# Performance work log

Hardware: AMD Instinct MI355X
Metric: run time of the kernel (lower is better)

The kernel has to match this reference:

```python
import jax, jax.numpy as jnp
import numpy as np

EPS = 1e-6  # flax nnx LayerNorm default

def _ln(x):
    # LayerNorm without scale/bias
    m = jnp.mean(x, axis=-1, keepdims=True)
    v = jnp.mean(jnp.square(x - m), axis=-1, keepdims=True)
    return (x - m) * jax.lax.rsqrt(v + EPS)

def _modulate(x, shift, scale):
    return x * (1.0 + scale[:, None]) + shift[:, None]

def setup_inputs() -> dict:
    key = jax.random.key(0)
    B, S, H, NH = 8, 1024, 1024, 16
    ks = jax.random.split(key, 12)
    s = lambda k, sh: jax.random.normal(k, sh, dtype=jnp.float32) * 0.02
    return {
        "x": jax.random.normal(ks[0], (B, S, H), dtype=jnp.float32),
        "c": jax.random.normal(ks[1], (B, H), dtype=jnp.float32),
        "w_ada": s(ks[2], (H, 6 * H)),
        "b_ada": jnp.zeros((6 * H,), dtype=jnp.float32),
        "w_qkv": s(ks[3], (H, 3 * H)),
        "w_proj": s(ks[4], (H, H)),
        "b_proj": jnp.zeros((H,), dtype=jnp.float32),
        "w_mlp1": s(ks[5], (H, 4 * H)),
        "b_mlp1": jnp.zeros((4 * H,), dtype=jnp.float32),
        "w_mlp2": s(ks[6], (4 * H, H)),
        "b_mlp2": jnp.zeros((H,), dtype=jnp.float32),
    }

def reference(x, c, w_ada, b_ada, w_qkv, w_proj, b_proj, w_mlp1, b_mlp1, w_mlp2, b_mlp2):
    B, S, H = x.shape
    NH = 16
    CH = H // NH
    # adaLN modulation: silu -> Linear
    cmod = jax.nn.silu(c) @ w_ada + b_ada  # [B, 6H]
    shift_msa, scale_msa, gate_msa, shift_mlp, scale_mlp, gate_mlp = jnp.split(cmod, 6, axis=-1)
    # attention branch
    x_mod = _modulate(_ln(x), shift_msa, scale_msa)
    qkv = x_mod @ w_qkv  # [B, S, 3H]
    k, q, v = jnp.split(qkv, 3, axis=-1)  # note source order: k, q, v
    k = k.reshape(B, S, NH, CH)
    q = q.reshape(B, S, NH, CH)
    v = v.reshape(B, S, NH, CH)
    q = q / CH  # faithful: divide by head_dim (not sqrt)
    w = jnp.einsum('bqhc,bkhc->bhqk', q, k).astype(jnp.float32)
    w = jax.nn.softmax(w, axis=-1)
    y = jnp.einsum('bhqk,bkhc->bqhc', w, v).reshape(B, S, H)
    attn_x = y @ w_proj + b_proj
    x = x + gate_msa[:, None] * attn_x
    # MLP branch
    x_mod2 = _modulate(_ln(x), shift_mlp, scale_mlp)
    h = jax.nn.gelu(x_mod2 @ w_mlp1 + b_mlp1)
    mlp_x = h @ w_mlp2 + b_mlp2
    x = x + gate_mlp[:, None] * mlp_x
    return x
```

## Files before the change

kernel.cpp:

```cpp
#include <hip/hip_runtime.h>
#include <stdint.h>

typedef unsigned short u16;
using bf16x8 = __attribute__((ext_vector_type(8))) __bf16;
using f32x4  = __attribute__((ext_vector_type(4))) float;

#define MFMA16(a,b,c) __builtin_amdgcn_mfma_f32_16x16x32_bf16((a),(b),(c),0,0,0)

__device__ __forceinline__ u16 f2bf(float f) {
  union { float f; uint32_t u; } v; v.f = f;
  uint32_t r = v.u + 0x7FFFu + ((v.u >> 16) & 1u);
  return (u16)(r >> 16);
}

__device__ __forceinline__ void gload_lds16(const void* g, void* l) {
  typedef const __attribute__((address_space(1))) void* gp_t;
  typedef __attribute__((address_space(3))) void* lp_t;
  __builtin_amdgcn_global_load_lds((gp_t)(uintptr_t)g,
                                   (lp_t)(uint32_t)(uintptr_t)l, 16, 0, 0);
}

__global__ __launch_bounds__(256)
void adaln_part_k(const float* __restrict__ c, const float* __restrict__ w,
                  float* __restrict__ partial) {
  const int jb = blockIdx.x, ks = blockIdx.y;
  const int j = jb * 256 + threadIdx.x;
  __shared__ float sil[8][32];
  {
    int b = threadIdx.x >> 5, kk = threadIdx.x & 31;
    float v = c[b * 1024 + ks * 32 + kk];
    sil[b][kk] = v / (1.f + __expf(-v));
  }
  __syncthreads();
  float acc[8] = {0,0,0,0,0,0,0,0};
#pragma unroll 8
  for (int kk = 0; kk < 32; ++kk) {
    float wv = w[(size_t)(ks * 32 + kk) * 6144 + j];
#pragma unroll
    for (int b = 0; b < 8; ++b) acc[b] += sil[b][kk] * wv;
  }
#pragma unroll
  for (int b = 0; b < 8; ++b)
    partial[((size_t)ks * 8 + b) * 6144 + j] = acc[b];
}

__global__ __launch_bounds__(256)
void adaln_red_k(const float* __restrict__ partial, const float* __restrict__ bias,
                 float* __restrict__ cmod) {
  int g = blockIdx.x * 256 + threadIdx.x;
  int j = g % 6144;
  float s = bias[j];
#pragma unroll 8
  for (int ks = 0; ks < 32; ++ks)
    s += partial[(size_t)ks * 8 * 6144 + g];
  cmod[g] = s;
}

__global__ __launch_bounds__(256)
void tcast_k(const float* __restrict__ in, u16* __restrict__ out, int K, int N,
             int lo, int hi, float scale) {
  __shared__ u16 t[64][65];
  int n0 = blockIdx.x * 64, k0 = blockIdx.y * 64;
#pragma unroll
  for (int i = 0; i < 16; ++i) {
    int idx = i * 256 + threadIdx.x;
    int r = idx >> 6, cc = idx & 63;
    float v = in[(size_t)(k0 + r) * N + n0 + cc];
    int n = n0 + cc;
    if (n >= lo && n < hi) v *= scale;
    t[r][cc] = f2bf(v);
  }
  __syncthreads();
#pragma unroll
  for (int i = 0; i < 16; ++i) {
    int idx = i * 256 + threadIdx.x;
    int r = idx >> 6, cc = idx & 63;
    out[(size_t)(n0 + r) * K + k0 + cc] = t[cc][r];
  }
}

__global__ __launch_bounds__(256)
void lnmod_k(const float* __restrict__ x, const float* __restrict__ cmod,
             int shift_off, int scale_off, u16* __restrict__ out) {
  int row = blockIdx.x;
  int b = row >> 10;
  const float4* xr = (const float4*)(x + (size_t)row * 1024);
  float4 v = xr[threadIdx.x];
  float s = v.x + v.y + v.z + v.w;
  float sq = v.x * v.x + v.y * v.y + v.z * v.z + v.w * v.w;
#pragma unroll
  for (int m = 32; m >= 1; m >>= 1) {
    s  += __shfl_xor(s, m);
    sq += __shfl_xor(sq, m);
  }
  __shared__ float ss[4], ssq[4];
  int wave = threadIdx.x >> 6, lane = threadIdx.x & 63;
  if (lane == 0) { ss[wave] = s; ssq[wave] = sq; }
  __syncthreads();
  s  = ss[0] + ss[1] + ss[2] + ss[3];
  sq = ssq[0] + ssq[1] + ssq[2] + ssq[3];
  float mean = s * (1.f / 1024.f);
  float var  = sq * (1.f / 1024.f) - mean * mean;
  float rstd = rsqrtf(var + 1e-6f);
  int col = threadIdx.x * 4;
  const float* sh = cmod + (size_t)b * 6144 + shift_off + col;
  const float* sc = cmod + (size_t)b * 6144 + scale_off + col;
  float xv[4] = {v.x, v.y, v.z, v.w};
  union { u16 o[4]; uint64_t u; } pk;
#pragma unroll
  for (int j = 0; j < 4; ++j)
    pk.o[j] = f2bf((xv[j] - mean) * rstd * (1.f + sc[j]) + sh[j]);
  *(uint64_t*)(out + (size_t)row * 1024 + col) = pk.u;
}

__global__ __launch_bounds__(256)
void tv_k(const u16* __restrict__ qkv, u16* __restrict__ vt) {
  __shared__ u16 t[64][65];
  int r0 = blockIdx.x * 64;
  int h = blockIdx.y;
  int b = r0 >> 10;
  int s0 = r0 & 1023;
#pragma unroll
  for (int i = 0; i < 16; ++i) {
    int idx = i * 256 + threadIdx.x;
    int r = idx >> 6, cc = idx & 63;
    t[r][cc] = qkv[(size_t)(r0 + r) * 3072 + 2048 + h * 64 + cc];
  }
  __syncthreads();
#pragma unroll
  for (int i = 0; i < 16; ++i) {
    int idx = i * 256 + threadIdx.x;
    int ch = idx >> 6, scc = idx & 63;
    vt[((size_t)(b * 16 + h) * 64 + ch) * 1024 + s0 + scc] = t[scc][ch];
  }
}

__device__ __forceinline__ float gelu_f(float x) {
  float z = 1.5957691216057308f * (x + 0.044715f * x * x * x);
  return x / (1.f + __expf(-z));
}

template <int EP>
__global__ __launch_bounds__(256)
void gemm_k(const u16* __restrict__ A, const u16* __restrict__ Bt,
            int N, int K,
            const float* __restrict__ bias, const float* __restrict__ resid,
            const float* __restrict__ gate, void* __restrict__ outp) {
  __shared__ __align__(16) u16 lds[2][2][128 * 32];
  const int nwg = gridDim.x * gridDim.y;
  int bid = blockIdx.y * gridDim.x + blockIdx.x;
  int swz = (bid & 7) * (nwg >> 3) + (bid >> 3);
  const int bn = swz % gridDim.x, bm = swz / gridDim.x;
  const int tid = threadIdx.x;
  const int wave = tid >> 6, lane = tid & 63;
  const int l15 = lane & 15, lhi = lane >> 4;
  const int wr = wave >> 1, wc = wave & 1;
  f32x4 acc[4][4] = {};
  const int nkt = K >> 5;
  const size_t arow0 = (size_t)bm * 128;
  const size_t brow0 = (size_t)bn * 128;

  auto stage = [&](int buf, int kt) {
#pragma unroll
    for (int i = 0; i < 2; ++i) {
      int c = (i * 4 + wave) * 64 + lane;
      int row = c >> 2;
      int kc = (c & 3) ^ ((row >> 1) & 3);
      gload_lds16(A  + (arow0 + row) * K + (size_t)kt * 32 + kc * 8,
                  &lds[buf][0][(i * 4 + wave) * 512]);
      gload_lds16(Bt + (brow0 + row) * K + (size_t)kt * 32 + kc * 8,
                  &lds[buf][1][(i * 4 + wave) * 512]);
    }
  };

  stage(0, 0);
  __syncthreads();
  for (int kt = 0; kt < nkt; ++kt) {
    int cur = kt & 1;
    if (kt + 1 < nkt) stage(cur ^ 1, kt + 1);
    bf16x8 af[4], bfr[4];
#pragma unroll
    for (int m = 0; m < 4; ++m) {
      int r = wr * 64 + m * 16 + l15;
      af[m] = *(const bf16x8*)&lds[cur][0][r * 32 + (lhi ^ ((r >> 1) & 3)) * 8];
    }
#pragma unroll
    for (int n = 0; n < 4; ++n) {
      int r = wc * 64 + n * 16 + l15;
      bfr[n] = *(const bf16x8*)&lds[cur][1][r * 32 + (lhi ^ ((r >> 1) & 3)) * 8];
    }
#pragma unroll
    for (int m = 0; m < 4; ++m)
#pragma unroll
      for (int n = 0; n < 4; ++n)
        acc[m][n] = MFMA16(af[m], bfr[n], acc[m][n]);
    __syncthreads();
  }

#pragma unroll
  for (int m = 0; m < 4; ++m) {
    int row = bm * 128 + wr * 64 + m * 16 + lhi * 4;
#pragma unroll
    for (int n = 0; n < 4; ++n) {
      int col = bn * 128 + wc * 64 + n * 16 + l15;
#pragma unroll
      for (int r = 0; r < 4; ++r) {
        int rr = row + r;
        float v = acc[m][n][r];
        if (EP == 0) {
          ((u16*)outp)[(size_t)rr * N + col] = f2bf(v);
        } else if (EP == 1) {
          ((u16*)outp)[(size_t)rr * N + col] = f2bf(gelu_f(v + bias[col]));
        } else {
          float t = v + bias[col];
          int b = rr >> 10;
          float res = resid[(size_t)rr * N + col];
          ((float*)outp)[(size_t)rr * N + col] = res + gate[(size_t)b * 6144 + col] * t;
        }
      }
    }
  }
}

__global__ __launch_bounds__(256)
void attn_k(const u16* __restrict__ qkv, const u16* __restrict__ vt,
            u16* __restrict__ y) {
  int bid0 = blockIdx.x + 16 * (blockIdx.y + 16 * blockIdx.z);
  int swz = (bid0 & 7) * 256 + (bid0 >> 3);
  const int qt = swz & 15, h = (swz >> 4) & 15, b = swz >> 8;
  const int tid = threadIdx.x, wave = tid >> 6, lane = tid & 63;
  const int l15 = lane & 15, lhi = lane >> 4;
  __shared__ __align__(16) u16 Qs[64 * 64];
  __shared__ __align__(16) u16 Ks[2][64 * 64];
  __shared__ __align__(16) u16 Vs[2][64 * 64];
  __shared__ __align__(16) u16 Ps[64 * 64];
  const size_t qrow0 = (size_t)b * 1024 + qt * 64;
  const size_t krow0 = (size_t)b * 1024;
  const size_t vrow0 = (size_t)(b * 16 + h) * 64;

  auto stageQ = [&]() {
#pragma unroll
    for (int i = 0; i < 2; ++i) {
      int c = (i * 4 + wave) * 64 + lane;
      int r = c >> 3, j = (c & 7) ^ (c >> 3 & 7);
      gload_lds16(qkv + (qrow0 + r) * 3072 + 1024 + h * 64 + j * 8,
                  &Qs[(i * 4 + wave) * 512]);
    }
  };
  auto stageKV = [&](int buf, int kt) {
#pragma unroll
    for (int i = 0; i < 2; ++i) {
      int c = (i * 4 + wave) * 64 + lane;
      int r = c >> 3, j = (c & 7) ^ (c >> 3 & 7);
      gload_lds16(qkv + (krow0 + kt * 64 + r) * 3072 + h * 64 + j * 8,
                  &Ks[buf][(i * 4 + wave) * 512]);
      gload_lds16(vt + (vrow0 + r) * 1024 + kt * 64 + j * 8,
                  &Vs[buf][(i * 4 + wave) * 512]);
    }
  };
  auto ldb = [](const u16* base, int row, int cc) -> bf16x8 {
    return *(const bf16x8*)&base[row * 64 + ((cc ^ (row & 7)) << 3)];
  };

  stageQ();
  stageKV(0, 0);
  __syncthreads();
  bf16x8 qf[2];
  qf[0] = ldb(Qs, wave * 16 + l15, lhi);
  qf[1] = ldb(Qs, wave * 16 + l15, 4 + lhi);

  bf16x8 ones;
#pragma unroll
  for (int j = 0; j < 8; ++j) ones[j] = (__bf16)1.0f;

  float m_r[4];
  f32x4 o[5] = {};
#pragma unroll
  for (int r = 0; r < 4; ++r) m_r[r] = -3.0e38f;

  for (int kt = 0; kt < 16; ++kt) {
    int cur = kt & 1;
    if (kt < 15) stageKV(cur ^ 1, kt + 1);
    f32x4 sf[4] = {};
    __builtin_amdgcn_s_setprio(1);
#pragma unroll
    for (int n = 0; n < 4; ++n) {
      bf16x8 k0 = ldb(Ks[cur], n * 16 + l15, lhi);
      bf16x8 k1 = ldb(Ks[cur], n * 16 + l15, 4 + lhi);
      sf[n] = MFMA16(qf[0], k0, sf[n]);
      sf[n] = MFMA16(qf[1], k1, sf[n]);
    }
    __builtin_amdgcn_s_setprio(0);
#pragma unroll
    for (int r = 0; r < 4; ++r) {
      float mx = fmaxf(fmaxf(sf[0][r], sf[1][r]), fmaxf(sf[2][r], sf[3][r]));
      mx = fmaxf(mx, __shfl_xor(mx, 1));
      mx = fmaxf(mx, __shfl_xor(mx, 2));
      mx = fmaxf(mx, __shfl_xor(mx, 4));
      mx = fmaxf(mx, __shfl_xor(mx, 8));
      float mn = fmaxf(m_r[r], mx);
      float al = __expf(m_r[r] - mn);
      m_r[r] = mn;
      float p0 = __expf(sf[0][r] - mn);
      float p1 = __expf(sf[1][r] - mn);
      float p2 = __expf(sf[2][r] - mn);
      float p3 = __expf(sf[3][r] - mn);
      o[0][r] *= al; o[1][r] *= al; o[2][r] *= al; o[3][r] *= al; o[4][r] *= al;
      int row = wave * 16 + lhi * 4 + r;
      int rb = row * 64, sw = (row & 7) << 3;
      Ps[rb + (l15 ^ sw)]        = f2bf(p0);
      Ps[rb + ((l15 + 16) ^ sw)] = f2bf(p1);
      Ps[rb + ((l15 + 32) ^ sw)] = f2bf(p2);
      Ps[rb + ((l15 + 48) ^ sw)] = f2bf(p3);
    }
    bf16x8 pf0 = ldb(Ps, wave * 16 + l15, lhi);
    bf16x8 pf1 = ldb(Ps, wave * 16 + l15, 4 + lhi);
    __builtin_amdgcn_s_setprio(1);
#pragma unroll
    for (int n = 0; n < 4; ++n) {
      bf16x8 v0 = ldb(Vs[cur], n * 16 + l15, lhi);
      bf16x8 v1 = ldb(Vs[cur], n * 16 + l15, 4 + lhi);
      o[n] = MFMA16(pf0, v0, o[n]);
      o[n] = MFMA16(pf1, v1, o[n]);
    }
    o[4] = MFMA16(pf0, ones, o[4]);
    o[4] = MFMA16(pf1, ones, o[4]);
    __builtin_amdgcn_s_setprio(0);
    __syncthreads();
  }
#pragma unroll
  for (int r = 0; r < 4; ++r) {
    float inv = 1.0f / o[4][r];
    size_t yrow = (qrow0 + wave * 16 + lhi * 4 + r) * 1024 + h * 64 + l15;
    y[yrow]      = f2bf(o[0][r] * inv);
    y[yrow + 16] = f2bf(o[1][r] * inv);
    y[yrow + 32] = f2bf(o[2][r] * inv);
    y[yrow + 48] = f2bf(o[3][r] * inv);
  }
}

extern "C" void kernel_launch(void* const* d_in, const int* in_sizes, int n_in,
                              void* d_out, int out_size, void* d_ws, size_t ws_size,
                              hipStream_t stream) {
  const float* x      = (const float*)d_in[0];
  const float* c      = (const float*)d_in[1];
  const float* w_ada  = (const float*)d_in[2];
  const float* b_ada  = (const float*)d_in[3];
  const float* w_qkv  = (const float*)d_in[4];
  const float* w_proj = (const float*)d_in[5];
  const float* b_proj = (const float*)d_in[6];
  const float* w_mlp1 = (const float*)d_in[7];
  const float* b_mlp1 = (const float*)d_in[8];
  const float* w_mlp2 = (const float*)d_in[9];
  const float* b_mlp2 = (const float*)d_in[10];
  float* out = (float*)d_out;

  char* ws = (char*)d_ws;
  size_t off = 0;
  auto alloc = [&](size_t bytes) {
    void* p = ws + off;
    off += (bytes + 255) & ~(size_t)255;
    return p;
  };
  float* cmod  = (float*)alloc((size_t)8 * 6144 * 4);
  float* apart = (float*)alloc((size_t)32 * 8 * 6144 * 4);
  u16* wqkvT   = (u16*)alloc((size_t)3072 * 1024 * 2);
  u16* wprojT  = (u16*)alloc((size_t)1024 * 1024 * 2);
  u16* wmlp1T  = (u16*)alloc((size_t)4096 * 1024 * 2);
  u16* wmlp2T  = (u16*)alloc((size_t)1024 * 4096 * 2);
  u16* xmod    = (u16*)alloc((size_t)8192 * 1024 * 2);
  u16* qkv     = (u16*)alloc((size_t)8192 * 3072 * 2);
  u16* vt      = (u16*)alloc((size_t)8 * 16 * 64 * 1024 * 2);
  float* x1    = (float*)alloc((size_t)8192 * 1024 * 4);
  u16* hbuf    = (u16*)alloc((size_t)8192 * 4096 * 2);
  u16* ybuf  = xmod;
  u16* xmod2 = qkv;

  adaln_part_k<<<dim3(24, 32), 256, 0, stream>>>(c, w_ada, apart);
  adaln_red_k<<<192, 256, 0, stream>>>(apart, b_ada, cmod);
  tcast_k<<<dim3(3072 / 64, 1024 / 64), 256, 0, stream>>>(w_qkv,  wqkvT,  1024, 3072,
                                                          1024, 2048, 1.0f / 64.0f);
  tcast_k<<<dim3(1024 / 64, 1024 / 64), 256, 0, stream>>>(w_proj, wprojT, 1024, 1024, 0, 0, 1.f);
  tcast_k<<<dim3(4096 / 64, 1024 / 64), 256, 0, stream>>>(w_mlp1, wmlp1T, 1024, 4096, 0, 0, 1.f);
  tcast_k<<<dim3(1024 / 64, 4096 / 64), 256, 0, stream>>>(w_mlp2, wmlp2T, 4096, 1024, 0, 0, 1.f);
  lnmod_k<<<8192, 256, 0, stream>>>(x, cmod, 0, 1024, xmod);
  gemm_k<0><<<dim3(3072 / 128, 8192 / 128), 256, 0, stream>>>(
      xmod, wqkvT, 3072, 1024, nullptr, nullptr, nullptr, qkv);
  tv_k<<<dim3(128, 16), 256, 0, stream>>>(qkv, vt);
  attn_k<<<dim3(16, 16, 8), 256, 0, stream>>>(qkv, vt, ybuf);
  gemm_k<2><<<dim3(1024 / 128, 8192 / 128), 256, 0, stream>>>(
      ybuf, wprojT, 1024, 1024, b_proj, x, cmod + 2048, x1);
  lnmod_k<<<8192, 256, 0, stream>>>(x1, cmod, 3072, 4096, xmod2);
  gemm_k<1><<<dim3(4096 / 128, 8192 / 128), 256, 0, stream>>>(
      xmod2, wmlp1T, 4096, 1024, b_mlp1, nullptr, nullptr, hbuf);
  gemm_k<2><<<dim3(1024 / 128, 8192 / 128), 256, 0, stream>>>(
      hbuf, wmlp2T, 1024, 4096, b_mlp2, x1, cmod + 5120, out);
}
```

Before: 409.4 us.

## Add 256x128 tile GEMM kernel for QKV and MLP GEMMs, drop block swizzle

Adds a gemm2_k variant in which each 256-thread block computes a 256x128 output tile, each wave holding 8x4 MFMA accumulators. It is used for the QKV, MLP1 and MLP2 GEMMs. The goal is more arithmetic per byte of LDS traffic, better operand reuse, and fewer blocks. The grouped block-index swizzle is also removed from the original gemm_k, so tiles launch in plain row-major order, which may hurt L2 locality. The larger tile raises register pressure (launch_bounds 256,2) and halves the block count, which could reduce occupancy or leave part of the GPU idle for the smaller N=1024 GEMM.

```diff
diff --git a/kernel.cpp b/kernel.cpp
--- a/kernel.cpp
+++ b/kernel.cpp
@@ -141,16 +141,99 @@
 }
 
 template <int EP>
+__global__ __launch_bounds__(256, 2)
+void gemm2_k(const u16* __restrict__ A, const u16* __restrict__ Bt,
+             int N, int K,
+             const float* __restrict__ bias, const float* __restrict__ resid,
+             const float* __restrict__ gate, void* __restrict__ outp) {
+  __shared__ __align__(16) u16 As[2][256 * 32];
+  __shared__ __align__(16) u16 Bs[2][128 * 32];
+  const int bn = blockIdx.x, bm = blockIdx.y;
+  const int tid = threadIdx.x;
+  const int wave = tid >> 6, lane = tid & 63;
+  const int l15 = lane & 15, lhi = lane >> 4;
+  const int wr = wave >> 1, wc = wave & 1;
+  f32x4 acc[8][4] = {};
+  const int nkt = K >> 5;
+  const size_t arow0 = (size_t)bm * 256;
+  const size_t brow0 = (size_t)bn * 128;
+
+  auto stage = [&](int buf, int kt) {
+#pragma unroll
+    for (int i = 0; i < 4; ++i) {
+      int q = (i * 4 + wave) * 64 + lane;
+      int row = q >> 2;
+      int kc = (q & 3) ^ ((row >> 1) & 3);
+      gload_lds16(A + (arow0 + row) * K + (size_t)kt * 32 + kc * 8,
+                  &As[buf][(i * 4 + wave) * 512]);
+    }
+#pragma unroll
+    for (int i = 0; i < 2; ++i) {
+      int q = (i * 4 + wave) * 64 + lane;
+      int row = q >> 2;
+      int kc = (q & 3) ^ ((row >> 1) & 3);
+      gload_lds16(Bt + (brow0 + row) * K + (size_t)kt * 32 + kc * 8,
+                  &Bs[buf][(i * 4 + wave) * 512]);
+    }
+  };
+
+  stage(0, 0);
+  __syncthreads();
+  for (int kt = 0; kt < nkt; ++kt) {
+    int cur = kt & 1;
+    if (kt + 1 < nkt) stage(cur ^ 1, kt + 1);
+    bf16x8 af[8], bfr[4];
+#pragma unroll
+    for (int m = 0; m < 8; ++m) {
+      int r = wr * 128 + m * 16 + l15;
+      af[m] = *(const bf16x8*)&As[cur][r * 32 + (lhi ^ ((r >> 1) & 3)) * 8];
+    }
+#pragma unroll
+    for (int n = 0; n < 4; ++n) {
+      int r = wc * 64 + n * 16 + l15;
+      bfr[n] = *(const bf16x8*)&Bs[cur][r * 32 + (lhi ^ ((r >> 1) & 3)) * 8];
+    }
+#pragma unroll
+    for (int m = 0; m < 8; ++m)
+#pragma unroll
+      for (int n = 0; n < 4; ++n)
+        acc[m][n] = MFMA16(af[m], bfr[n], acc[m][n]);
+    __syncthreads();
+  }
+
+#pragma unroll
+  for (int m = 0; m < 8; ++m) {
+    int row = bm * 256 + wr * 128 + m * 16 + lhi * 4;
+#pragma unroll
+    for (int n = 0; n < 4; ++n) {
+      int col = bn * 128 + wc * 64 + n * 16 + l15;
+#pragma unroll
+      for (int r = 0; r < 4; ++r) {
+        int rr = row + r;
+        float v = acc[m][n][r];
+        if (EP == 0) {
+          ((u16*)outp)[(size_t)rr * N + col] = f2bf(v);
+        } else if (EP == 1) {
+          ((u16*)outp)[(size_t)rr * N + col] = f2bf(gelu_f(v + bias[col]));
+        } else {
+          float t = v + bias[col];
+          int b = rr >> 10;
+          float res = resid[(size_t)rr * N + col];
+          ((float*)outp)[(size_t)rr * N + col] = res + gate[(size_t)b * 6144 + col] * t;
+        }
+      }
+    }
+  }
+}
+
+template <int EP>
 __global__ __launch_bounds__(256)
 void gemm_k(const u16* __restrict__ A, const u16* __restrict__ Bt,
             int N, int K,
             const float* __restrict__ bias, const float* __restrict__ resid,
             const float* __restrict__ gate, void* __restrict__ outp) {
   __shared__ __align__(16) u16 lds[2][2][128 * 32];
-  const int nwg = gridDim.x * gridDim.y;
-  int bid = blockIdx.y * gridDim.x + blockIdx.x;
-  int swz = (bid & 7) * (nwg >> 3) + (bid >> 3);
-  const int bn = swz % gridDim.x, bm = swz / gridDim.x;
+  const int bn = blockIdx.x, bm = blockIdx.y;
   const int tid = threadIdx.x;
   const int wave = tid >> 6, lane = tid & 63;
   const int l15 = lane & 15, lhi = lane >> 4;
@@ -384,15 +467,15 @@
   tcast_k<<<dim3(4096 / 64, 1024 / 64), 256, 0, stream>>>(w_mlp1, wmlp1T, 1024, 4096, 0, 0, 1.f);
   tcast_k<<<dim3(1024 / 64, 4096 / 64), 256, 0, stream>>>(w_mlp2, wmlp2T, 4096, 1024, 0, 0, 1.f);
   lnmod_k<<<8192, 256, 0, stream>>>(x, cmod, 0, 1024, xmod);
-  gemm_k<0><<<dim3(3072 / 128, 8192 / 128), 256, 0, stream>>>(
+  gemm2_k<0><<<dim3(3072 / 128, 8192 / 256), 256, 0, stream>>>(
       xmod, wqkvT, 3072, 1024, nullptr, nullptr, nullptr, qkv);
   tv_k<<<dim3(128, 16), 256, 0, stream>>>(qkv, vt);
   attn_k<<<dim3(16, 16, 8), 256, 0, stream>>>(qkv, vt, ybuf);
   gemm_k<2><<<dim3(1024 / 128, 8192 / 128), 256, 0, stream>>>(
       ybuf, wprojT, 1024, 1024, b_proj, x, cmod + 2048, x1);
   lnmod_k<<<8192, 256, 0, stream>>>(x1, cmod, 3072, 4096, xmod2);
-  gemm_k<1><<<dim3(4096 / 128, 8192 / 128), 256, 0, stream>>>(
+  gemm2_k<1><<<dim3(4096 / 128, 8192 / 256), 256, 0, stream>>>(
       xmod2, wmlp1T, 4096, 1024, b_mlp1, nullptr, nullptr, hbuf);
-  gemm_k<2><<<dim3(1024 / 128, 8192 / 128), 256, 0, stream>>>(
+  gemm2_k<2><<<dim3(1024 / 128, 8192 / 256), 256, 0, stream>>>(
       hbuf, wmlp2T, 1024, 4096, b_mlp2, x1, cmod + 5120, out);
 }
```

Measured after the change: 435.3 us. +6.3%, slower.

## Double attention query tile to 128 rows per block to reuse K/V tiles

Applied to the files above, without the earlier changes.

The attention kernel now processes 128 query rows per block (two 16-row groups per wave) instead of 64, halving the grid and the number of times each K/V tile is loaded from global memory into LDS. Each K/V tile staged into shared memory is reused across twice as many query rows, cutting global/L2 traffic and barrier count per unit of work. In exchange, register use (two sets of accumulators and softmax state) and LDS grow, and the grid shrinks to 1024 blocks, which may lower occupancy or latency hiding.

```diff
diff --git a/kernel.cpp b/kernel.cpp
--- a/kernel.cpp
+++ b/kernel.cpp
@@ -225,33 +225,33 @@
 __global__ __launch_bounds__(256)
 void attn_k(const u16* __restrict__ qkv, const u16* __restrict__ vt,
             u16* __restrict__ y) {
-  int bid0 = blockIdx.x + 16 * (blockIdx.y + 16 * blockIdx.z);
-  int swz = (bid0 & 7) * 256 + (bid0 >> 3);
-  const int qt = swz & 15, h = (swz >> 4) & 15, b = swz >> 8;
+  int bid0 = blockIdx.x + 8 * (blockIdx.y + 16 * blockIdx.z);
+  int swz = (bid0 & 7) * 128 + (bid0 >> 3);
+  const int qt = swz & 7, h = (swz >> 3) & 15, b = swz >> 7;
   const int tid = threadIdx.x, wave = tid >> 6, lane = tid & 63;
   const int l15 = lane & 15, lhi = lane >> 4;
-  __shared__ __align__(16) u16 Qs[64 * 64];
+  __shared__ __align__(16) u16 Qs[128 * 64];
   __shared__ __align__(16) u16 Ks[2][64 * 64];
   __shared__ __align__(16) u16 Vs[2][64 * 64];
-  __shared__ __align__(16) u16 Ps[64 * 64];
-  const size_t qrow0 = (size_t)b * 1024 + qt * 64;
+  __shared__ __align__(16) u16 Ps[128 * 64];
+  const size_t qrow0 = (size_t)b * 1024 + qt * 128;
   const size_t krow0 = (size_t)b * 1024;
   const size_t vrow0 = (size_t)(b * 16 + h) * 64;
 
   auto stageQ = [&]() {
 #pragma unroll
+    for (int i = 0; i < 4; ++i) {
+      int c = (i * 4 + wave) * 64 + lane;
+      int r = c >> 3, j = (c & 7) ^ (r & 7);
+      gload_lds16(qkv + (qrow0 + r) * 3072 + 1024 + h * 64 + j * 8,
+                  &Qs[(i * 4 + wave) * 512]);
+    }
+  };
+  auto stageKV = [&](int buf, int kt) {
+#pragma unroll
     for (int i = 0; i < 2; ++i) {
       int c = (i * 4 + wave) * 64 + lane;
-      int r = c >> 3, j = (c & 7) ^ (c >> 3 & 7);
-      gload_lds16(qkv + (qrow0 + r) * 3072 + 1024 + h * 64 + j * 8,
-                  &Qs[(i * 4 + wave) * 512]);
-    }
-  };
-  auto stageKV = [&](int buf, int kt) {
-#pragma unroll
-    for (int i = 0; i < 2; ++i) {
-      int c = (i * 4 + wave) * 64 + lane;
-      int r = c >> 3, j = (c & 7) ^ (c >> 3 & 7);
+      int r = c >> 3, j = (c & 7) ^ (r & 7);
       gload_lds16(qkv + (krow0 + kt * 64 + r) * 3072 + h * 64 + j * 8,
                   &Ks[buf][(i * 4 + wave) * 512]);
       gload_lds16(vt + (vrow0 + r) * 1024 + kt * 64 + j * 8,
@@ -265,78 +265,90 @@
   stageQ();
   stageKV(0, 0);
   __syncthreads();
-  bf16x8 qf[2];
-  qf[0] = ldb(Qs, wave * 16 + l15, lhi);
-  qf[1] = ldb(Qs, wave * 16 + l15, 4 + lhi);
+  bf16x8 qf[2][2];
+#pragma unroll
+  for (int g = 0; g < 2; ++g) {
+    int r = wave * 32 + g * 16 + l15;
+    qf[g][0] = ldb(Qs, r, lhi);
+    qf[g][1] = ldb(Qs, r, 4 + lhi);
+  }
 
   bf16x8 ones;
 #pragma unroll
   for (int j = 0; j < 8; ++j) ones[j] = (__bf16)1.0f;
 
-  float m_r[4];
-  f32x4 o[5] = {};
-#pragma unroll
-  for (int r = 0; r < 4; ++r) m_r[r] = -3.0e38f;
+  float m_r[2][4];
+  f32x4 o[2][5] = {};
+#pragma unroll
+  for (int g = 0; g < 2; ++g)
+#pragma unroll
+    for (int r = 0; r < 4; ++r) m_r[g][r] = -3.0e38f;
 
   for (int kt = 0; kt < 16; ++kt) {
     int cur = kt & 1;
     if (kt < 15) stageKV(cur ^ 1, kt + 1);
-    f32x4 sf[4] = {};
-    __builtin_amdgcn_s_setprio(1);
-#pragma unroll
-    for (int n = 0; n < 4; ++n) {
-      bf16x8 k0 = ldb(Ks[cur], n * 16 + l15, lhi);
-      bf16x8 k1 = ldb(Ks[cur], n * 16 + l15, 4 + lhi);
-      sf[n] = MFMA16(qf[0], k0, sf[n]);
-      sf[n] = MFMA16(qf[1], k1, sf[n]);
-    }
-    __builtin_amdgcn_s_setprio(0);
+#pragma unroll
+    for (int g = 0; g < 2; ++g) {
+      f32x4 sf[4] = {};
+      __builtin_amdgcn_s_setprio(1);
+#pragma unroll
+      for (int n = 0; n < 4; ++n) {
+        bf16x8 k0 = ldb(Ks[cur], n * 16 + l15, lhi);
+        bf16x8 k1 = ldb(Ks[cur], n * 16 + l15, 4 + lhi);
+        sf[n] = MFMA16(qf[g][0], k0, sf[n]);
+        sf[n] = MFMA16(qf[g][1], k1, sf[n]);
+      }
+      __builtin_amdgcn_s_setprio(0);
+#pragma unroll
+      for (int r = 0; r < 4; ++r) {
+        float mx = fmaxf(fmaxf(sf[0][r], sf[1][r]), fmaxf(sf[2][r], sf[3][r]));
+        mx = fmaxf(mx, __shfl_xor(mx, 1));
+        mx = fmaxf(mx, __shfl_xor(mx, 2));
+        mx = fmaxf(mx, __shfl_xor(mx, 4));
+        mx = fmaxf(mx, __shfl_xor(mx, 8));
+        float mn = fmaxf(m_r[g][r], mx);
+        float al = __expf(m_r[g][r] - mn);
+        m_r[g][r] = mn;
+        float p0 = __expf(sf[0][r] - mn);
+        float p1 = __expf(sf[1][r] - mn);
+        float p2 = __expf(sf[2][r] - mn);
+        float p3 = __expf(sf[3][r] - mn);
+        o[g][0][r] *= al; o[g][1][r] *= al; o[g][2][r] *= al;
+        o[g][3][r] *= al; o[g][4][r] *= al;
+        int row = wave * 32 + g * 16 + lhi * 4 + r;
+        int rb = row * 64, sw = (row & 7) << 3;
+        Ps[rb + (l15 ^ sw)]        = f2bf(p0);
+        Ps[rb + ((l15 + 16) ^ sw)] = f2bf(p1);
+        Ps[rb + ((l15 + 32) ^ sw)] = f2bf(p2);
+        Ps[rb + ((l15 + 48) ^ sw)] = f2bf(p3);
+      }
+      bf16x8 pf0 = ldb(Ps, wave * 32 + g * 16 + l15, lhi);
+      bf16x8 pf1 = ldb(Ps, wave * 32 + g * 16 + l15, 4 + lhi);
+      __builtin_amdgcn_s_setprio(1);
+#pragma unroll
+      for (int n = 0; n < 4; ++n) {
+        bf16x8 v0 = ldb(Vs[cur], n * 16 + l15, lhi);
+        bf16x8 v1 = ldb(Vs[cur], n * 16 + l15, 4 + lhi);
+        o[g][n] = MFMA16(pf0, v0, o[g][n]);
+        o[g][n] = MFMA16(pf1, v1, o[g][n]);
+      }
+      o[g][4] = MFMA16(pf0, ones, o[g][4]);
+      o[g][4] = MFMA16(pf1, ones, o[g][4]);
+      __builtin_amdgcn_s_setprio(0);
+    }
+    __syncthreads();
+  }
+#pragma unroll
+  for (int g = 0; g < 2; ++g)
 #pragma unroll
     for (int r = 0; r < 4; ++r) {
-      float mx = fmaxf(fmaxf(sf[0][r], sf[1][r]), fmaxf(sf[2][r], sf[3][r]));
-      mx = fmaxf(mx, __shfl_xor(mx, 1));
-      mx = fmaxf(mx, __shfl_xor(mx, 2));
-      mx = fmaxf(mx, __shfl_xor(mx, 4));
-      mx = fmaxf(mx, __shfl_xor(mx, 8));
-      float mn = fmaxf(m_r[r], mx);
-      float al = __expf(m_r[r] - mn);
-      m_r[r] = mn;
-      float p0 = __expf(sf[0][r] - mn);
-      float p1 = __expf(sf[1][r] - mn);
-      float p2 = __expf(sf[2][r] - mn);
-      float p3 = __expf(sf[3][r] - mn);
-      o[0][r] *= al; o[1][r] *= al; o[2][r] *= al; o[3][r] *= al; o[4][r] *= al;
-      int row = wave * 16 + lhi * 4 + r;
-      int rb = row * 64, sw = (row & 7) << 3;
-      Ps[rb + (l15 ^ sw)]        = f2bf(p0);
-      Ps[rb + ((l15 + 16) ^ sw)] = f2bf(p1);
-      Ps[rb + ((l15 + 32) ^ sw)] = f2bf(p2);
-      Ps[rb + ((l15 + 48) ^ sw)] = f2bf(p3);
-    }
-    bf16x8 pf0 = ldb(Ps, wave * 16 + l15, lhi);
-    bf16x8 pf1 = ldb(Ps, wave * 16 + l15, 4 + lhi);
-    __builtin_amdgcn_s_setprio(1);
-#pragma unroll
-    for (int n = 0; n < 4; ++n) {
-      bf16x8 v0 = ldb(Vs[cur], n * 16 + l15, lhi);
-      bf16x8 v1 = ldb(Vs[cur], n * 16 + l15, 4 + lhi);
-      o[n] = MFMA16(pf0, v0, o[n]);
-      o[n] = MFMA16(pf1, v1, o[n]);
-    }
-    o[4] = MFMA16(pf0, ones, o[4]);
-    o[4] = MFMA16(pf1, ones, o[4]);
-    __builtin_amdgcn_s_setprio(0);
-    __syncthreads();
-  }
-#pragma unroll
-  for (int r = 0; r < 4; ++r) {
-    float inv = 1.0f / o[4][r];
-    size_t yrow = (qrow0 + wave * 16 + lhi * 4 + r) * 1024 + h * 64 + l15;
-    y[yrow]      = f2bf(o[0][r] * inv);
-    y[yrow + 16] = f2bf(o[1][r] * inv);
-    y[yrow + 32] = f2bf(o[2][r] * inv);
-    y[yrow + 48] = f2bf(o[3][r] * inv);
-  }
+      float inv = 1.0f / o[g][4][r];
+      size_t yrow = (qrow0 + wave * 32 + g * 16 + lhi * 4 + r) * 1024 + h * 64 + l15;
+      y[yrow]      = f2bf(o[g][0][r] * inv);
+      y[yrow + 16] = f2bf(o[g][1][r] * inv);
+      y[yrow + 32] = f2bf(o[g][2][r] * inv);
+      y[yrow + 48] = f2bf(o[g][3][r] * inv);
+    }
 }
 
 extern "C" void kernel_launch(void* const* d_in, const int* in_sizes, int n_in,
@@ -387,7 +399,7 @@
   gemm_k<0><<<dim3(3072 / 128, 8192 / 128), 256, 0, stream>>>(
       xmod, wqkvT, 3072, 1024, nullptr, nullptr, nullptr, qkv);
   tv_k<<<dim3(128, 16), 256, 0, stream>>>(qkv, vt);
-  attn_k<<<dim3(16, 16, 8), 256, 0, stream>>>(qkv, vt, ybuf);
+  attn_k<<<dim3(8, 16, 8), 256, 0, stream>>>(qkv, vt, ybuf);
   gemm_k<2><<<dim3(1024 / 128, 8192 / 128), 256, 0, stream>>>(
       ybuf, wprojT, 1024, 1024, b_proj, x, cmod + 2048, x1);
   lnmod_k<<<8192, 256, 0, stream>>>(x1, cmod, 3072, 4096, xmod2);
```

Result: no change. 416.6 us (+1.8%).
